# Optimization experiments

Hardware: AMD Instinct MI355X
Metric: run time of the kernel (lower is better)

## Reference

```python
import jax, jax.numpy as jnp
import numpy as np

EPS = 1e-3  # batch_norm_epsilon


def _lstm_last(xs, W, U, b):
    """Keras-order LSTM (gates i,f,g,o); returns last hidden state [B,H]."""
    B = xs.shape[0]
    H = U.shape[0]

    def step(carry, xt):
        h, c = carry
        z = xt @ W + h @ U + b  # [B, 4H]
        i, f, g, o = jnp.split(z, 4, axis=-1)
        i = jax.nn.sigmoid(i)
        f = jax.nn.sigmoid(f)
        g = jnp.tanh(g)
        o = jax.nn.sigmoid(o)
        c = f * c + i * g
        h = o * jnp.tanh(c)
        return (h, c), None

    init = (jnp.zeros((B, H), xs.dtype), jnp.zeros((B, H), xs.dtype))
    (h, _), _ = jax.lax.scan(step, init, jnp.swapaxes(xs, 0, 1))
    return h


def setup_inputs() -> dict:
    key = jax.random.key(0)
    ks = jax.random.split(key, 10)
    B, T, C, H = 32, 512, 512, 512
    s_in = 1.0 / np.sqrt(C)
    s_rec = 1.0 / np.sqrt(H)
    return {
        "x": jax.random.normal(ks[0], (B, T, C), jnp.float32),
        # BatchNorm params (inference / moving stats)
        "gamma": jnp.ones((C,), jnp.float32),
        "beta": jnp.zeros((C,), jnp.float32),
        "moving_mean": jax.random.normal(ks[1], (C,), jnp.float32) * 0.1,
        "moving_var": jnp.abs(jax.random.normal(ks[2], (C,), jnp.float32)) * 0.1 + 1.0,
        # forward-direction LSTM
        "Wf": jax.random.normal(ks[3], (C, 4 * H), jnp.float32) * s_in,
        "Uf": jax.random.normal(ks[4], (H, 4 * H), jnp.float32) * s_rec,
        "bf": jnp.zeros((4 * H,), jnp.float32),
        # backward-direction LSTM
        "Wb": jax.random.normal(ks[5], (C, 4 * H), jnp.float32) * s_in,
        "Ub": jax.random.normal(ks[6], (H, 4 * H), jnp.float32) * s_rec,
        "bb": jnp.zeros((4 * H,), jnp.float32),
    }


def reference(x, gamma, beta, moving_mean, moving_var, Wf, Uf, bf, Wb, Ub, bb):
    # BatchNorm (inference) over last axis
    inv = jax.lax.rsqrt(moving_var + EPS)
    xn = (x - moving_mean) * inv * gamma + beta
    # Bidirectional LSTM, merge_mode='concat', return_sequences=False
    h_fwd = _lstm_last(xn, Wf, Uf, bf)
    h_bwd = _lstm_last(xn[:, ::-1, :], Wb, Ub, bb)
    return jnp.concatenate([h_fwd, h_bwd], axis=-1)  # [B, 2H]
```

## Files before the change

### kernel.cpp

```cpp
#include <hip/hip_runtime.h>
#include <stdint.h>

typedef __attribute__((ext_vector_type(8))) short short8;
typedef __attribute__((ext_vector_type(4))) float f32x4;
typedef __attribute__((ext_vector_type(2))) float f32x2;

#define NB 32
#define NBH 16
#define NT 512
#define NC 512
#define NH 512
#define NG 2048
#define WPG 16
#define NWG 64
#define UPW 32

__device__ __forceinline__ float bf2f(unsigned short u){
  union { unsigned int i; float f; } v; v.i = ((unsigned int)u) << 16; return v.f;
}
__device__ __forceinline__ unsigned short f2bf(float f){
  union { float f; unsigned int i; } v; v.f = f;
  unsigned int r = v.i + 0x7fffu + ((v.i >> 16) & 1u);
  return (unsigned short)(r >> 16);
}
__device__ __forceinline__ bool dt_fp32(const void* gamma){
  return ((const unsigned short*)gamma)[0] != 0x3F80;
}
__device__ __forceinline__ float ldv(const void* p, size_t i, bool f32){
  return f32 ? ((const float*)p)[i] : bf2f(((const unsigned short*)p)[i]);
}
__device__ __forceinline__ short8 frag_from_f32(const float* p){
  short8 r;
  #pragma unroll
  for (int j = 0; j < 8; ++j) r[j] = (short)f2bf(p[j]);
  return r;
}
__device__ __forceinline__ float sigm(float x){ return 1.f/(1.f + __expf(-x)); }
__device__ __forceinline__ float tanh_(float x){ return 1.f - 2.f/(1.f + __expf(2.f*x)); }

__device__ __forceinline__ unsigned int llc_load_u32(const unsigned int* p){
  unsigned int r;
  asm volatile("global_load_dword %0, %1, off sc0 sc1\n\ts_waitcnt vmcnt(0)"
               : "=v"(r) : "v"(p) : "memory");
  return r;
}
__device__ __forceinline__ void llc_store_u32(unsigned int* p, unsigned int v){
  asm volatile("global_store_dword %0, %1, off sc0 sc1" :: "v"(p), "v"(v) : "memory");
}
__device__ __forceinline__ void llc_load_hfrags4(const unsigned short* p0, short8 hf[4]){
  asm volatile(
    "global_load_dwordx4 %0, %4, off sc0 sc1\n\t"
    "global_load_dwordx4 %1, %4, off offset:64 sc0 sc1\n\t"
    "global_load_dwordx4 %2, %4, off offset:128 sc0 sc1\n\t"
    "global_load_dwordx4 %3, %4, off offset:192 sc0 sc1\n\t"
    "s_waitcnt vmcnt(0)"
    : "=&v"(hf[0]), "=&v"(hf[1]), "=&v"(hf[2]), "=&v"(hf[3])
    : "v"(p0) : "memory");
}

__global__ void k_init(const void* __restrict__ gamma,
                       const void* __restrict__ beta,
                       const void* __restrict__ mmean,
                       const void* __restrict__ mvar,
                       float* __restrict__ scale, float* __restrict__ shift,
                       unsigned short* __restrict__ hbuf, unsigned int* __restrict__ flags){
  bool f32 = dt_fp32(gamma);
  int tid = blockIdx.x * 256 + threadIdx.x;
  if (blockIdx.x == 0){
    for (int c = threadIdx.x; c < NC; c += 256){
      float s = ldv(gamma, c, f32) * rsqrtf(ldv(mvar, c, f32) + 1e-3f);
      scale[c] = s;
      shift[c] = ldv(beta, c, f32) - ldv(mmean, c, f32) * s;
    }
    if (threadIdx.x < 128) flags[threadIdx.x] = 0u;
  }
  for (int i = tid; i < 4*2*NBH*NH; i += gridDim.x * 256) hbuf[i] = 0;
}

__global__ void k_xcast(const void* __restrict__ x, const void* __restrict__ gamma,
                        unsigned short* __restrict__ x2){
  bool f32 = dt_fp32(gamma);
  int i = blockIdx.x * 256 + threadIdx.x;
  int c8 = i & 63;
  int rest = i >> 6;
  int t = rest & (NT - 1);
  int b = rest >> 9;
  size_t src = ((size_t)b * NT + t) * NC + c8 * 8;
  size_t dst = ((size_t)t * NB + b) * NC + c8 * 8;
  unsigned int pk[4];
  if (f32){
    const float* p = (const float*)x + src;
    #pragma unroll
    for (int j = 0; j < 4; ++j)
      pk[j] = (unsigned int)f2bf(p[2*j]) | ((unsigned int)f2bf(p[2*j+1]) << 16);
  } else {
    __builtin_memcpy(pk, (const unsigned short*)x + src, 16);
  }
  __builtin_memcpy(x2 + dst, pk, 16);
}

__global__ __launch_bounds__(256, 1) void k_lstm(
    const void* __restrict__ x, const unsigned short* __restrict__ x2, int use_x2,
    const void* __restrict__ Wf, const void* __restrict__ Uf,
    const void* __restrict__ Wb, const void* __restrict__ Ub,
    const void* __restrict__ bfv, const void* __restrict__ bbv,
    const void* __restrict__ gamma,
    const float* __restrict__ scale, const float* __restrict__ shift,
    unsigned short* __restrict__ hbuf, unsigned int* __restrict__ flags,
    void* __restrict__ out){
  __shared__ float zbuf[4][NBH][132];
  __shared__ float fscr[256];
  __shared__ float fb[128];

  bool f32 = dt_fp32(gamma);
  int wg   = blockIdx.x;
  int dir  = wg & 1;
  int half = (wg >> 1) & 1;
  int wgd  = wg >> 2;
  int gidx = wg & 3;
  int ubase = wgd * UPW;
  const void* W = dir ? Wb : Wf;
  const void* U = dir ? Ub : Uf;
  const void* bvec = dir ? bbv : bfv;
  int tid  = threadIdx.x;
  int lane = tid & 63, wave = tid >> 6;
  int m = lane & 15, q = lane >> 4;

  short8 bw[4][8], bu[4][8];
  #pragma unroll
  for (int kcl = 0; kcl < 4; ++kcl){
    int kc = wave * 4 + kcl;
    #pragma unroll
    for (int nt = 0; nt < 8; ++nt){
      int col = (nt >> 1) * NH + ubase + (nt & 1) * 16 + m;
      short8 vw, vu;
      #pragma unroll
      for (int j = 0; j < 8; ++j){
        int k = kc * 32 + q * 8 + j;
        vu[j] = (short)f2bf(ldv(U, (size_t)k * NG + col, f32));
        vw[j] = (short)f2bf(scale[k] * ldv(W, (size_t)k * NG + col, f32));
      }
      bw[kcl][nt] = vw; bu[kcl][nt] = vu;
    }
  }

  {
    int cidx = tid >> 1, kh = tid & 1;
    int col = (cidx >> 5) * NH + ubase + (cidx & 31);
    float a = 0.f;
    for (int k = kh * 256; k < kh * 256 + 256; ++k)
      a += shift[k] * ldv(W, (size_t)k * NG + col, f32);
    fscr[tid] = a;
    __syncthreads();
    if (tid < 128)
      fb[tid] = fscr[2*tid] + fscr[2*tid+1]
              + ldv(bvec, (tid >> 5) * NH + ubase + (tid & 31), f32);
    __syncthreads();
  }

  int pb = tid >> 4, pu2 = (tid & 15) * 2;
  float bias_r[2][4];
  #pragma unroll
  for (int j = 0; j < 2; ++j)
    #pragma unroll
    for (int g = 0; g < 4; ++g) bias_r[j][g] = fb[g * 32 + pu2 + j];
  float cst[2] = {0.f, 0.f};

  unsigned int* gflags  = flags + gidx * 32;
  unsigned int* ownflag = gflags + wgd;
  unsigned short* hb0 = hbuf + (size_t)gidx * 2 * NBH * NH;

  short8 xf[4];
  {
    int tt0 = dir ? (NT - 1) : 0;
    int b = half * 16 + m;
    #pragma unroll
    for (int kcl = 0; kcl < 4; ++kcl){
      int kc = wave * 4 + kcl;
      if (use_x2){
        size_t xi = ((size_t)tt0 * NB + b) * NC + kc * 32 + q * 8;
        __builtin_memcpy(&xf[kcl], x2 + xi, 16);
      } else {
        size_t xi = ((size_t)b * NT + tt0) * NC + kc * 32 + q * 8;
        if (f32) xf[kcl] = frag_from_f32((const float*)x + xi);
        else     __builtin_memcpy(&xf[kcl], (const unsigned short*)x + xi, 16);
      }
    }
  }

  #pragma unroll 1
  for (int t = 0; t < NT; ++t){
    const unsigned short* hcur = hb0 + (size_t)(t & 1) * NBH * NH;
    unsigned short* hnext = hb0 + (size_t)((t + 1) & 1) * NBH * NH;

    f32x4 acc[8];
    #pragma unroll
    for (int nt = 0; nt < 8; ++nt) acc[nt] = (f32x4){0.f,0.f,0.f,0.f};

    #pragma unroll
    for (int kcl = 0; kcl < 4; ++kcl)
      #pragma unroll
      for (int nt = 0; nt < 8; ++nt)
        acc[nt] = __builtin_amdgcn_mfma_f32_16x16x32_bf16(xf[kcl], bw[kcl][nt], acc[nt], 0, 0, 0);

    if (t < NT - 1){
      int ttn = dir ? (NT - 2 - t) : (t + 1);
      int b = half * 16 + m;
      #pragma unroll
      for (int kcl = 0; kcl < 4; ++kcl){
        int kc = wave * 4 + kcl;
        if (use_x2){
          size_t xi = ((size_t)ttn * NB + b) * NC + kc * 32 + q * 8;
          __builtin_memcpy(&xf[kcl], x2 + xi, 16);
        } else {
          size_t xi = ((size_t)b * NT + ttn) * NC + kc * 32 + q * 8;
          if (f32) xf[kcl] = frag_from_f32((const float*)x + xi);
          else     __builtin_memcpy(&xf[kcl], (const unsigned short*)x + xi, 16);
        }
      }
    }

    if (t > 0){
      unsigned int tgt = (unsigned int)t;
      while (true){
        unsigned int v = llc_load_u32(gflags + (lane & 15));
        if (__all((int)(v >= tgt))) break;
      }
    }

    short8 hf[4];
    llc_load_hfrags4(hcur + (size_t)m * NH + wave * 128 + q * 8, hf);
    #pragma unroll
    for (int kcl = 0; kcl < 4; ++kcl)
      #pragma unroll
      for (int nt = 0; nt < 8; ++nt)
        acc[nt] = __builtin_amdgcn_mfma_f32_16x16x32_bf16(hf[kcl], bu[kcl][nt], acc[nt], 0, 0, 0);

    #pragma unroll
    for (int nt = 0; nt < 8; ++nt){
      int cb = (nt >> 1) * 32 + (nt & 1) * 16 + m;
      #pragma unroll
      for (int r = 0; r < 4; ++r)
        zbuf[wave][q * 4 + r][cb] = acc[nt][r];
    }
    __syncthreads();

    float z[2][4];
    #pragma unroll
    for (int g = 0; g < 4; ++g){ z[0][g] = bias_r[0][g]; z[1][g] = bias_r[1][g]; }
    #pragma unroll
    for (int w = 0; w < 4; ++w)
      #pragma unroll
      for (int g = 0; g < 4; ++g){
        f32x2 v = *(const f32x2*)&zbuf[w][pb][g * 32 + pu2];
        z[0][g] += v[0]; z[1][g] += v[1];
      }
    float hv[2];
    #pragma unroll
    for (int j = 0; j < 2; ++j){
      float iv = sigm(z[j][0]), fv = sigm(z[j][1]), gv = tanh_(z[j][2]), ov = sigm(z[j][3]);
      cst[j] = fv * cst[j] + iv * gv;
      hv[j] = ov * tanh_(cst[j]);
    }

    if (t == NT - 1){
      size_t o0 = (size_t)(half * 16 + pb) * (2 * NH) + dir * NH + ubase + pu2;
      if (f32){
        f32x2 ov2 = {hv[0], hv[1]};
        *(f32x2*)&((float*)out)[o0] = ov2;
      } else {
        unsigned int pk = (unsigned int)f2bf(hv[0]) | ((unsigned int)f2bf(hv[1]) << 16);
        *(unsigned int*)&((unsigned short*)out)[o0] = pk;
      }
      break;
    }

    {
      unsigned int pk = (unsigned int)f2bf(hv[0]) | ((unsigned int)f2bf(hv[1]) << 16);
      llc_store_u32((unsigned int*)(hnext + (size_t)pb * NH + ubase + pu2), pk);
    }

    __syncthreads();
    if (tid == 0) llc_store_u32(ownflag, (unsigned int)(t + 1));
  }
}

extern "C" void kernel_launch(void* const* d_in, const int* in_sizes, int n_in,
                              void* d_out, int out_size, void* d_ws, size_t ws_size,
                              hipStream_t stream){
  const void* x     = d_in[0];
  const void* gamma = d_in[1];
  const void* beta  = d_in[2];
  const void* mmean = d_in[3];
  const void* mvar  = d_in[4];
  const void* Wf    = d_in[5];
  const void* Uf    = d_in[6];
  const void* bfv   = d_in[7];
  const void* Wb    = d_in[8];
  const void* Ub    = d_in[9];
  const void* bbv   = d_in[10];

  char* ws = (char*)d_ws;
  float* scale = (float*)(ws + 0);
  float* shift = (float*)(ws + 2048);
  unsigned short* hbuf = (unsigned short*)(ws + 20480);
  unsigned int* flags  = (unsigned int*)(ws + 20480 + 131072);
  size_t x2_off = 20480 + 131072 + 4096;
  unsigned short* x2 = (unsigned short*)(ws + x2_off);
  size_t x2_bytes = (size_t)NT * NB * NC * 2;
  int use_x2 = (ws_size >= x2_off + x2_bytes) ? 1 : 0;

  hipLaunchKernelGGL(k_init, dim3(64),  dim3(256), 0, stream,
                     gamma, beta, mmean, mvar, scale, shift, hbuf, flags);
  if (use_x2)
    hipLaunchKernelGGL(k_xcast, dim3((NB*NT*NC/8)/256), dim3(256), 0, stream,
                       x, gamma, x2);
  hipLaunchKernelGGL(k_lstm, dim3(NWG), dim3(256), 0, stream,
                     x, x2, use_x2, Wf, Uf, Wb, Ub, bfv, bbv, gamma, scale, shift,
                     hbuf, flags, d_out);
}
```

Baseline: 1.853 ms.

## Replace per-step flag barrier with tagged hidden-state words and adaptive backoff

Each bf16 hidden value is now stored in a 32-bit word whose low 16 bits hold the timestep tag. Consumers poll the h-buffer directly until every tag matches, instead of spinning on per-workgroup flags and then loading h. This removes the block-wide __syncthreads and the separate flag store/load round trip from the recurrent critical path. The cost is double the h-buffer traffic and repeated full reloads when polling fails. An adaptive spin delay tuned with s_memrealtime is added to cut down on failed polls.

```diff
diff --git a/kernel.cpp b/kernel.cpp
--- a/kernel.cpp
+++ b/kernel.cpp
@@ -4,6 +4,8 @@
 typedef __attribute__((ext_vector_type(8))) short short8;
 typedef __attribute__((ext_vector_type(4))) float f32x4;
 typedef __attribute__((ext_vector_type(2))) float f32x2;
+typedef __attribute__((ext_vector_type(4))) unsigned int u32x4;
+typedef __attribute__((ext_vector_type(2))) unsigned int u32x2;
 
 #define NB 32
 #define NBH 16
@@ -38,24 +40,28 @@
 __device__ __forceinline__ float sigm(float x){ return 1.f/(1.f + __expf(-x)); }
 __device__ __forceinline__ float tanh_(float x){ return 1.f - 2.f/(1.f + __expf(2.f*x)); }
 
-__device__ __forceinline__ unsigned int llc_load_u32(const unsigned int* p){
-  unsigned int r;
-  asm volatile("global_load_dword %0, %1, off sc0 sc1\n\ts_waitcnt vmcnt(0)"
-               : "=v"(r) : "v"(p) : "memory");
-  return r;
-}
-__device__ __forceinline__ void llc_store_u32(unsigned int* p, unsigned int v){
-  asm volatile("global_store_dword %0, %1, off sc0 sc1" :: "v"(p), "v"(v) : "memory");
-}
-__device__ __forceinline__ void llc_load_hfrags4(const unsigned short* p0, short8 hf[4]){
+__device__ __forceinline__ unsigned int permhi(unsigned int hi, unsigned int lo){
+  return __builtin_amdgcn_perm(hi, lo, 0x07060302u);
+}
+
+__device__ __forceinline__ void tag_load(const unsigned int* p0, u32x4 r[8]){
   asm volatile(
-    "global_load_dwordx4 %0, %4, off sc0 sc1\n\t"
-    "global_load_dwordx4 %1, %4, off offset:64 sc0 sc1\n\t"
-    "global_load_dwordx4 %2, %4, off offset:128 sc0 sc1\n\t"
-    "global_load_dwordx4 %3, %4, off offset:192 sc0 sc1\n\t"
+    "global_load_dwordx4 %0, %8, off sc0 sc1\n\t"
+    "global_load_dwordx4 %1, %8, off offset:16 sc0 sc1\n\t"
+    "global_load_dwordx4 %2, %8, off offset:128 sc0 sc1\n\t"
+    "global_load_dwordx4 %3, %8, off offset:144 sc0 sc1\n\t"
+    "global_load_dwordx4 %4, %8, off offset:256 sc0 sc1\n\t"
+    "global_load_dwordx4 %5, %8, off offset:272 sc0 sc1\n\t"
+    "global_load_dwordx4 %6, %8, off offset:384 sc0 sc1\n\t"
+    "global_load_dwordx4 %7, %8, off offset:400 sc0 sc1\n\t"
     "s_waitcnt vmcnt(0)"
-    : "=&v"(hf[0]), "=&v"(hf[1]), "=&v"(hf[2]), "=&v"(hf[3])
+    : "=&v"(r[0]), "=&v"(r[1]), "=&v"(r[2]), "=&v"(r[3]),
+      "=&v"(r[4]), "=&v"(r[5]), "=&v"(r[6]), "=&v"(r[7])
     : "v"(p0) : "memory");
+}
+__device__ __forceinline__ void tag_store(unsigned int* p, unsigned int lo, unsigned int hi){
+  u32x2 v; v[0] = lo; v[1] = hi;
+  asm volatile("global_store_dwordx2 %0, %1, off sc0 sc1" :: "v"(p), "v"(v) : "memory");
 }
 
 __global__ void k_init(const void* __restrict__ gamma,
@@ -63,7 +69,7 @@
                        const void* __restrict__ mmean,
                        const void* __restrict__ mvar,
                        float* __restrict__ scale, float* __restrict__ shift,
-                       unsigned short* __restrict__ hbuf, unsigned int* __restrict__ flags){
+                       unsigned int* __restrict__ hbuf){
   bool f32 = dt_fp32(gamma);
   int tid = blockIdx.x * 256 + threadIdx.x;
   if (blockIdx.x == 0){
@@ -72,9 +78,8 @@
       scale[c] = s;
       shift[c] = ldv(beta, c, f32) - ldv(mmean, c, f32) * s;
     }
-    if (threadIdx.x < 128) flags[threadIdx.x] = 0u;
-  }
-  for (int i = tid; i < 4*2*NBH*NH; i += gridDim.x * 256) hbuf[i] = 0;
+  }
+  for (int i = tid; i < 4*2*NBH*NH; i += gridDim.x * 256) hbuf[i] = 0u;
 }
 
 __global__ void k_xcast(const void* __restrict__ x, const void* __restrict__ gamma,
@@ -106,8 +111,7 @@
     const void* __restrict__ bfv, const void* __restrict__ bbv,
     const void* __restrict__ gamma,
     const float* __restrict__ scale, const float* __restrict__ shift,
-    unsigned short* __restrict__ hbuf, unsigned int* __restrict__ flags,
-    void* __restrict__ out){
+    unsigned int* __restrict__ hbuf, void* __restrict__ out){
   __shared__ float zbuf[4][NBH][132];
   __shared__ float fscr[256];
   __shared__ float fb[128];
@@ -166,9 +170,7 @@
     for (int g = 0; g < 4; ++g) bias_r[j][g] = fb[g * 32 + pu2 + j];
   float cst[2] = {0.f, 0.f};
 
-  unsigned int* gflags  = flags + gidx * 32;
-  unsigned int* ownflag = gflags + wgd;
-  unsigned short* hb0 = hbuf + (size_t)gidx * 2 * NBH * NH;
+  unsigned int* hb32 = hbuf + (size_t)gidx * 2 * NBH * NH;
 
   short8 xf[4];
   {
@@ -188,10 +190,12 @@
     }
   }
 
+  int dly = 100;
+
   #pragma unroll 1
   for (int t = 0; t < NT; ++t){
-    const unsigned short* hcur = hb0 + (size_t)(t & 1) * NBH * NH;
-    unsigned short* hnext = hb0 + (size_t)((t + 1) & 1) * NBH * NH;
+    const unsigned int* hcur = hb32 + (size_t)(t & 1) * NBH * NH;
+    unsigned int* hnext = hb32 + (size_t)((t + 1) & 1) * NBH * NH;
 
     f32x4 acc[8];
     #pragma unroll
@@ -219,22 +223,47 @@
         }
       }
     }
-
-    if (t > 0){
-      unsigned int tgt = (unsigned int)t;
+    __builtin_amdgcn_sched_barrier(0);
+
+    u32x4 raw[8];
+    {
+      unsigned int tg = (unsigned int)t;
+      if (t > 0 && dly > 0){
+        unsigned long long t0 = __builtin_amdgcn_s_memrealtime();
+        while ((unsigned long long)(__builtin_amdgcn_s_memrealtime() - t0)
+               < (unsigned long long)dly) {}
+      }
+      const unsigned int* p0 = hcur + (size_t)m * NH + wave * 128 + q * 8;
+      int tries = 0;
       while (true){
-        unsigned int v = llc_load_u32(gflags + (lane & 15));
-        if (__all((int)(v >= tgt))) break;
-      }
-    }
-
-    short8 hf[4];
-    llc_load_hfrags4(hcur + (size_t)m * NH + wave * 128 + q * 8, hf);
-    #pragma unroll
-    for (int kcl = 0; kcl < 4; ++kcl)
+        tag_load(p0, raw);
+        unsigned int d = 0;
+        #pragma unroll
+        for (int i = 0; i < 8; ++i)
+          d |= (raw[i][0] ^ tg) | (raw[i][1] ^ tg) | (raw[i][2] ^ tg) | (raw[i][3] ^ tg);
+        if (__all((int)((d & 0xffffu) == 0u))) break;
+        ++tries;
+      }
+      if (t > 0){
+        dly += tries ? 20 : -1;
+        if (dly < 0) dly = 0;
+        if (dly > 300) dly = 300;
+      }
+    }
+
+    #pragma unroll
+    for (int kcl = 0; kcl < 4; ++kcl){
+      union { short8 s; unsigned int w[4]; } u;
+      u32x4 a = raw[2 * kcl];
+      u32x4 b = raw[2 * kcl + 1];
+      u.w[0] = permhi(a[1], a[0]);
+      u.w[1] = permhi(a[3], a[2]);
+      u.w[2] = permhi(b[1], b[0]);
+      u.w[3] = permhi(b[3], b[2]);
       #pragma unroll
       for (int nt = 0; nt < 8; ++nt)
-        acc[nt] = __builtin_amdgcn_mfma_f32_16x16x32_bf16(hf[kcl], bu[kcl][nt], acc[nt], 0, 0, 0);
+        acc[nt] = __builtin_amdgcn_mfma_f32_16x16x32_bf16(u.s, bu[kcl][nt], acc[nt], 0, 0, 0);
+    }
 
     #pragma unroll
     for (int nt = 0; nt < 8; ++nt){
@@ -276,12 +305,11 @@
     }
 
     {
-      unsigned int pk = (unsigned int)f2bf(hv[0]) | ((unsigned int)f2bf(hv[1]) << 16);
-      llc_store_u32((unsigned int*)(hnext + (size_t)pb * NH + ubase + pu2), pk);
-    }
-
-    __syncthreads();
-    if (tid == 0) llc_store_u32(ownflag, (unsigned int)(t + 1));
+      unsigned int tag1 = (unsigned int)(t + 1);
+      unsigned int w0 = ((unsigned int)f2bf(hv[0]) << 16) | tag1;
+      unsigned int w1 = ((unsigned int)f2bf(hv[1]) << 16) | tag1;
+      tag_store(hnext + (size_t)pb * NH + ubase + pu2, w0, w1);
+    }
   }
 }
 
@@ -303,19 +331,18 @@
   char* ws = (char*)d_ws;
   float* scale = (float*)(ws + 0);
   float* shift = (float*)(ws + 2048);
-  unsigned short* hbuf = (unsigned short*)(ws + 20480);
-  unsigned int* flags  = (unsigned int*)(ws + 20480 + 131072);
-  size_t x2_off = 20480 + 131072 + 4096;
+  unsigned int* hbuf = (unsigned int*)(ws + 20480);
+  size_t x2_off = 20480 + 262144 + 4096;
   unsigned short* x2 = (unsigned short*)(ws + x2_off);
   size_t x2_bytes = (size_t)NT * NB * NC * 2;
   int use_x2 = (ws_size >= x2_off + x2_bytes) ? 1 : 0;
 
   hipLaunchKernelGGL(k_init, dim3(64),  dim3(256), 0, stream,
-                     gamma, beta, mmean, mvar, scale, shift, hbuf, flags);
+                     gamma, beta, mmean, mvar, scale, shift, hbuf);
   if (use_x2)
     hipLaunchKernelGGL(k_xcast, dim3((NB*NT*NC/8)/256), dim3(256), 0, stream,
                        x, gamma, x2);
   hipLaunchKernelGGL(k_lstm, dim3(NWG), dim3(256), 0, stream,
                      x, x2, use_x2, Wf, Uf, Wb, Ub, bfv, bbv, gamma, scale, shift,
-                     hbuf, flags, d_out);
-}
+                     hbuf, d_out);
+}
```

Measured after the change: 2.002 ms. 8.0% more time.

## Poll barrier flags from one wave with pipelined loads; merge init into xcast

Applied to the files above, without the earlier changes.

The cross-workgroup step barrier now has a single wave poll the global flags, keeping two outstanding uncached loads in flight so polling latency is overlapped. The other waves spin on an LDS variable that the polling wave sets once all flags are ready. Separately, the init kernel is folded into the cast kernel, removing one launch. The LDS handoff adds intra-block ordering concerns, and the per-block memory traffic from polling goes down.

```diff
diff --git a/kernel.cpp b/kernel.cpp
--- a/kernel.cpp
+++ b/kernel.cpp
@@ -38,12 +38,6 @@
 __device__ __forceinline__ float sigm(float x){ return 1.f/(1.f + __expf(-x)); }
 __device__ __forceinline__ float tanh_(float x){ return 1.f - 2.f/(1.f + __expf(2.f*x)); }
 
-__device__ __forceinline__ unsigned int llc_load_u32(const unsigned int* p){
-  unsigned int r;
-  asm volatile("global_load_dword %0, %1, off sc0 sc1\n\ts_waitcnt vmcnt(0)"
-               : "=v"(r) : "v"(p) : "memory");
-  return r;
-}
 __device__ __forceinline__ void llc_store_u32(unsigned int* p, unsigned int v){
   asm volatile("global_store_dword %0, %1, off sc0 sc1" :: "v"(p), "v"(v) : "memory");
 }
@@ -58,14 +52,15 @@
     : "v"(p0) : "memory");
 }
 
-__global__ void k_init(const void* __restrict__ gamma,
-                       const void* __restrict__ beta,
-                       const void* __restrict__ mmean,
-                       const void* __restrict__ mvar,
-                       float* __restrict__ scale, float* __restrict__ shift,
-                       unsigned short* __restrict__ hbuf, unsigned int* __restrict__ flags){
+__global__ void k_xcast(const void* __restrict__ x, const void* __restrict__ gamma,
+                        const void* __restrict__ beta,
+                        const void* __restrict__ mmean,
+                        const void* __restrict__ mvar,
+                        float* __restrict__ scale, float* __restrict__ shift,
+                        unsigned short* __restrict__ hbuf, unsigned int* __restrict__ flags,
+                        unsigned short* __restrict__ x2, int do_x2){
   bool f32 = dt_fp32(gamma);
-  int tid = blockIdx.x * 256 + threadIdx.x;
+  int i = blockIdx.x * 256 + threadIdx.x;
   if (blockIdx.x == 0){
     for (int c = threadIdx.x; c < NC; c += 256){
       float s = ldv(gamma, c, f32) * rsqrtf(ldv(mvar, c, f32) + 1e-3f);
@@ -74,13 +69,8 @@
     }
     if (threadIdx.x < 128) flags[threadIdx.x] = 0u;
   }
-  for (int i = tid; i < 4*2*NBH*NH; i += gridDim.x * 256) hbuf[i] = 0;
-}
-
-__global__ void k_xcast(const void* __restrict__ x, const void* __restrict__ gamma,
-                        unsigned short* __restrict__ x2){
-  bool f32 = dt_fp32(gamma);
-  int i = blockIdx.x * 256 + threadIdx.x;
+  for (int k = i; k < 4*2*NBH*NH; k += gridDim.x * 256) hbuf[k] = 0;
+  if (!do_x2) return;
   int c8 = i & 63;
   int rest = i >> 6;
   int t = rest & (NT - 1);
@@ -111,6 +101,7 @@
   __shared__ float zbuf[4][NBH][132];
   __shared__ float fscr[256];
   __shared__ float fb[128];
+  __shared__ unsigned int go;
 
   bool f32 = dt_fp32(gamma);
   int wg   = blockIdx.x;
@@ -126,6 +117,8 @@
   int lane = tid & 63, wave = tid >> 6;
   int m = lane & 15, q = lane >> 4;
 
+  if (tid == 0) go = 0u;
+
   short8 bw[4][8], bu[4][8];
   #pragma unroll
   for (int kcl = 0; kcl < 4; ++kcl){
@@ -192,6 +185,7 @@
   for (int t = 0; t < NT; ++t){
     const unsigned short* hcur = hb0 + (size_t)(t & 1) * NBH * NH;
     unsigned short* hnext = hb0 + (size_t)((t + 1) & 1) * NBH * NH;
+    unsigned int fl0 = 0u, fl1 = 0u;
 
     f32x4 acc[8];
     #pragma unroll
@@ -222,14 +216,27 @@
 
     if (t > 0){
       unsigned int tgt = (unsigned int)t;
-      while (true){
-        unsigned int v = llc_load_u32(gflags + (lane & 15));
-        if (__all((int)(v >= tgt))) break;
+      if (wave == 0){
+        const unsigned int* fp = gflags + (lane & 15);
+        asm volatile("global_load_dword %0, %1, off sc0 sc1" : "=v"(fl0) : "v"(fp) : "memory");
+        asm volatile("global_load_dword %0, %1, off sc0 sc1" : "=v"(fl1) : "v"(fp) : "memory");
+        while (true){
+          asm volatile("s_waitcnt vmcnt(1)" : "+v"(fl0) :: "memory");
+          if (__all((int)(fl0 >= tgt))) break;
+          asm volatile("global_load_dword %0, %1, off sc0 sc1" : "=v"(fl0) : "v"(fp) : "memory");
+          asm volatile("s_waitcnt vmcnt(1)" : "+v"(fl1) :: "memory");
+          if (__all((int)(fl1 >= tgt))) break;
+          asm volatile("global_load_dword %0, %1, off sc0 sc1" : "=v"(fl1) : "v"(fp) : "memory");
+        }
+        if (lane == 0) *(volatile unsigned int*)&go = tgt;
+      } else {
+        while (*(volatile unsigned int*)&go < tgt) {}
       }
     }
 
     short8 hf[4];
     llc_load_hfrags4(hcur + (size_t)m * NH + wave * 128 + q * 8, hf);
+    asm volatile("" : "+v"(fl0), "+v"(fl1));
     #pragma unroll
     for (int kcl = 0; kcl < 4; ++kcl)
       #pragma unroll
@@ -310,11 +317,9 @@
   size_t x2_bytes = (size_t)NT * NB * NC * 2;
   int use_x2 = (ws_size >= x2_off + x2_bytes) ? 1 : 0;
 
-  hipLaunchKernelGGL(k_init, dim3(64),  dim3(256), 0, stream,
-                     gamma, beta, mmean, mvar, scale, shift, hbuf, flags);
-  if (use_x2)
-    hipLaunchKernelGGL(k_xcast, dim3((NB*NT*NC/8)/256), dim3(256), 0, stream,
-                       x, gamma, x2);
+  int xgrid = use_x2 ? (NB*NT*NC/8)/256 : 64;
+  hipLaunchKernelGGL(k_xcast, dim3(xgrid), dim3(256), 0, stream,
+                     x, gamma, beta, mmean, mvar, scale, shift, hbuf, flags, x2, use_x2);
   hipLaunchKernelGGL(k_lstm, dim3(NWG), dim3(256), 0, stream,
                      x, x2, use_x2, Wf, Uf, Wb, Ub, bfv, bbv, gamma, scale, shift,
                      hbuf, flags, d_out);
```

Measured after the change: 1.848 ms. Within noise of the previous version (-0.3%).
